# Kernel tuning notes

Hardware: AMD Instinct MI355X
Metric: run time of the kernel (lower is better)

The kernel has to match this reference:

```python
import jax, jax.numpy as jnp
import numpy as np

B, LQ, LK, D = 16, 2048, 2048, 64
TEMPERATURE = 8.0  # sqrt(d_k)


def setup_inputs() -> dict:
    key = jax.random.key(0)
    kq, kk, kv, km = jax.random.split(key, 4)
    q = jax.random.normal(kq, (B, LQ, D), dtype=jnp.float32)
    k = jax.random.normal(kk, (B, LK, D), dtype=jnp.float32)
    v = jax.random.normal(kv, (B, LK, D), dtype=jnp.float32)
    mask = jax.random.randint(km, (B, LQ, LK), 0, 2).astype(jnp.bool_)
    return {"q": q, "k": k, "v": v, "mask": mask}


def reference(q, k, v, mask):
    # attn = bmm(q, k^T) / temperature  -> [B, LQ, LK]
    attn = jnp.einsum("bqd,bkd->bqk", q, k) / TEMPERATURE
    attn = jnp.where(mask, -jnp.inf, attn)
    attn = jax.nn.softmax(attn, axis=2)
    out = jnp.einsum("bqk,bkd->bqd", attn, v)  # [B, LQ, D]
    return out, attn
```

## Files before the change

kernel.cpp:

```cpp
#include <hip/hip_runtime.h>
#include <hip/hip_bf16.h>

namespace {
constexpr int kB = 16;
constexpr int kLQ = 2048;
constexpr int kLK = 2048;
constexpr int kD = 64;
constexpr float kLog2e = 1.44269504088896340736f;
constexpr int kKStrB = 144;
constexpr int kMStrB = 136;
constexpr int kBStrB = 272;
constexpr int kChunk = 256;
constexpr int kEStrB = 528;
}

using short8 = __attribute__((ext_vector_type(8))) short;
using f32x4  = __attribute__((ext_vector_type(4))) float;

union S8U { short8 v; unsigned u[4]; };

static __device__ __forceinline__ unsigned pk2(float lo, float hi) {
    __hip_bfloat162 h = __float22bfloat162_rn(float2{lo, hi});
    unsigned short a = __builtin_bit_cast(unsigned short, h.x);
    unsigned short b = __builtin_bit_cast(unsigned short, h.y);
    return (unsigned)a | ((unsigned)b << 16);
}
static __device__ __forceinline__ float bf2f(unsigned short s) {
    unsigned u = ((unsigned)s) << 16;
    return __builtin_bit_cast(float, u);
}

__global__ __launch_bounds__(256, 6) void k1_fused(
    const float* __restrict__ qg, const float* __restrict__ kg,
    const void* __restrict__ maskg, unsigned short* __restrict__ ews,
    float* __restrict__ attng, float* __restrict__ outg)
{
    __shared__ __align__(16) unsigned char s_kst[128 * kKStrB];
    __shared__ __align__(16) unsigned char s_mst[16 * kMStrB];
    __shared__ __align__(16) unsigned char s_bnc[16 * kBStrB];
    __shared__ float s_wsum[4][16];
    __shared__ float s_rinv[16];
    __shared__ int s_flag;

    const int tid = threadIdx.x;
    const int wave = tid >> 6;
    const int lane = tid & 63;
    const int r16 = lane & 15;
    const int g = lane >> 4;

    const int blk = blockIdx.x;
    const int b = blk >> 7;
    const int qt = blk & 127;
    const size_t grow0 = (size_t)b * kLQ + qt * 16;

    if (tid < 64) {
        unsigned w = ((const unsigned*)maskg)[tid];
        unsigned long long bal = __ballot((w & 0xFFFFFF00u) != 0u);
        if (tid == 0) s_flag = (bal != 0ull) ? 1 : 0;
    }
    __syncthreads();
    const bool mask_byte = (s_flag != 0);
    const unsigned char* mask_u8 = (const unsigned char*)maskg;
    const int* mask_i32 = (const int*)maskg;

    short8 q0, q1;
    {
        const float4* qp = (const float4*)(qg + (grow0 + r16) * kD);
        const float s = 0.125f * kLog2e;
        float4 x0 = qp[2*g + 0], x1 = qp[2*g + 1];
        float4 x2 = qp[2*g + 8], x3 = qp[2*g + 9];
        x0 *= s; x1 *= s; x2 *= s; x3 *= s;
        S8U a, c;
        a.u[0] = pk2(x0.x, x0.y); a.u[1] = pk2(x0.z, x0.w);
        a.u[2] = pk2(x1.x, x1.y); a.u[3] = pk2(x1.z, x1.w);
        c.u[0] = pk2(x2.x, x2.y); c.u[1] = pk2(x2.z, x2.w);
        c.u[2] = pk2(x3.x, x3.y); c.u[3] = pk2(x3.z, x3.w);
        q0 = a.v; q1 = c.v;
    }

    float wsum = 0.f;

    for (int sub = 0; sub < kLK / 128; ++sub) {
        const int csub = sub * 128;
#pragma unroll
        for (int i = 0; i < 8; ++i) {
            const int row = (tid >> 4) + i * 16;
            const float4 y = *(const float4*)(kg + ((size_t)b * kLK + csub + row) * kD + (tid & 15) * 4);
            uint2 p{ pk2(y.x, y.y), pk2(y.z, y.w) };
            *(uint2*)(s_kst + row * kKStrB + (tid & 15) * 8) = p;
        }
        {
            const int mrow = tid >> 4;
            const int mseg = tid & 15;
            unsigned long long f;
            if (mask_byte) {
                f = *(const unsigned long long*)(mask_u8 + (grow0 + mrow) * kLK + csub + mseg * 8);
            } else {
                const int* mp = mask_i32 + (grow0 + mrow) * kLK + csub + mseg * 8;
                const int4 m0 = *(const int4*)mp;
                const int4 m1 = *(const int4*)(mp + 4);
                f  = (m0.x ? 1ull : 0ull)        | (m0.y ? 1ull << 8 : 0ull)
                   | (m0.z ? 1ull << 16 : 0ull)  | (m0.w ? 1ull << 24 : 0ull)
                   | (m1.x ? 1ull << 32 : 0ull)  | (m1.y ? 1ull << 40 : 0ull)
                   | (m1.z ? 1ull << 48 : 0ull)  | (m1.w ? 1ull << 56 : 0ull);
            }
            *(unsigned long long*)(s_mst + mrow * kMStrB + mseg * 8) = f;
        }
        __syncthreads();

        const unsigned char* kb = s_kst + (wave * 32 + r16) * kKStrB;
        const short8 kA0 = *(const short8*)(kb + g * 16);
        const short8 kA1 = *(const short8*)(kb + 64 + g * 16);
        const short8 kB0 = *(const short8*)(kb + 16 * kKStrB + g * 16);
        const short8 kB1 = *(const short8*)(kb + 16 * kKStrB + 64 + g * 16);
        f32x4 accA = {0.f, 0.f, 0.f, 0.f}, accB = {0.f, 0.f, 0.f, 0.f};
        accA = __builtin_amdgcn_mfma_f32_16x16x32_bf16(kA0, q0, accA, 0, 0, 0);
        accA = __builtin_amdgcn_mfma_f32_16x16x32_bf16(kA1, q1, accA, 0, 0, 0);
        accB = __builtin_amdgcn_mfma_f32_16x16x32_bf16(kB0, q0, accB, 0, 0, 0);
        accB = __builtin_amdgcn_mfma_f32_16x16x32_bf16(kB1, q1, accB, 0, 0, 0);

        const unsigned mwA = *(const unsigned*)(s_mst + r16 * kMStrB + wave * 32 + 4 * g);
        const unsigned mwB = *(const unsigned*)(s_mst + r16 * kMStrB + wave * 32 + 16 + 4 * g);
        float eA[4], eB[4];
#pragma unroll
        for (int r = 0; r < 4; ++r) {
            eA[r] = ((mwA >> (8*r)) & 0xFFu) ? 0.f : __builtin_amdgcn_exp2f(accA[r]);
            eB[r] = ((mwB >> (8*r)) & 0xFFu) ? 0.f : __builtin_amdgcn_exp2f(accB[r]);
        }
        wsum += (eA[0] + eA[1]) + (eA[2] + eA[3]) + (eB[0] + eB[1]) + (eB[2] + eB[3]);
        uint2 pA{ pk2(eA[0], eA[1]), pk2(eA[2], eA[3]) };
        uint2 pB{ pk2(eB[0], eB[1]), pk2(eB[2], eB[3]) };
        *(uint2*)(s_bnc + r16 * kBStrB + wave * 64 + 8 * g) = pA;
        *(uint2*)(s_bnc + r16 * kBStrB + wave * 64 + 32 + 8 * g) = pB;
        __syncthreads();

        {
            const int erow = tid >> 4;
            const int eseg = tid & 15;
            *(short8*)(ews + (grow0 + erow) * kLK + csub + eseg * 8) =
                *(const short8*)(s_bnc + erow * kBStrB + eseg * 16);
        }
    }

    wsum += __shfl_xor(wsum, 16, 64);
    wsum += __shfl_xor(wsum, 32, 64);
    if (g == 0) s_wsum[wave][r16] = wsum;
    __syncthreads();
    if (tid < 16) {
        const float rs = s_wsum[0][tid] + s_wsum[1][tid] + s_wsum[2][tid] + s_wsum[3][tid];
        outg[(grow0 + tid) * kD] = rs;
        s_rinv[tid] = __builtin_amdgcn_rcpf(rs);
    }
    __syncthreads();

#pragma unroll 2
    for (int r = 0; r < 16; ++r) {
        const float rinv = s_rinv[r];
        const short8 ev = *(const short8*)(ews + (grow0 + r) * kLK + tid * 8);
        f32x4 a0, a1;
        a0[0] = bf2f((unsigned short)ev[0]) * rinv;
        a0[1] = bf2f((unsigned short)ev[1]) * rinv;
        a0[2] = bf2f((unsigned short)ev[2]) * rinv;
        a0[3] = bf2f((unsigned short)ev[3]) * rinv;
        a1[0] = bf2f((unsigned short)ev[4]) * rinv;
        a1[1] = bf2f((unsigned short)ev[5]) * rinv;
        a1[2] = bf2f((unsigned short)ev[6]) * rinv;
        a1[3] = bf2f((unsigned short)ev[7]) * rinv;
        float* ap = attng + (grow0 + r) * kLK + tid * 8;
        *(f32x4*)ap = a0;
        *(f32x4*)(ap + 4) = a1;
    }
}

__global__ __launch_bounds__(512, 8) void k2_pv(
    const float* __restrict__ vg, const unsigned short* __restrict__ ews,
    float* __restrict__ outg)
{
    __shared__ __align__(16) unsigned char s_e[16 * kEStrB];
    __shared__ float s_red[16][kD];
    __shared__ float s_rinv[16];

    const int tid = threadIdx.x;
    const int wave = tid >> 6;
    const int lane = tid & 63;
    const int r16 = lane & 15;
    const int g = lane >> 4;

    const int blk = blockIdx.x;
    const int b = blk >> 7;
    const size_t grow0 = (size_t)b * kLQ + (blk & 127) * 16;

    if (tid < 16)
        s_rinv[tid] = __builtin_amdgcn_rcpf(outg[(grow0 + tid) * kD]);
    __syncthreads();

    const int d0 = (wave & 3) * 16;
    const int kh = wave >> 2;
    f32x4 acc = {0.f, 0.f, 0.f, 0.f};
    const float* vbase = vg + (size_t)b * kLK * kD + d0 + r16;

    for (int chunk = 0; chunk < kLK / kChunk; ++chunk) {
        const int c0 = chunk * kChunk;
        {
            const int row = tid >> 5;
            const int cc = tid & 31;
            const short8 ev = *(const short8*)(ews + (grow0 + row) * kLK + c0 + cc * 8);
            *(short8*)(s_e + row * kEStrB + cc * 16) = ev;
        }
        __syncthreads();
#pragma unroll
        for (int s = 0; s < 4; ++s) {
            const int kk = kh * 128 + s * 32 + 8 * g;
            const short8 af = *(const short8*)(s_e + r16 * kEStrB + kk * 2);
            const float* vp = vbase + (size_t)(c0 + kk) * kD;
            float v0 = vp[0*kD], v1 = vp[1*kD], v2 = vp[2*kD], v3 = vp[3*kD];
            float v4 = vp[4*kD], v5 = vp[5*kD], v6 = vp[6*kD], v7 = vp[7*kD];
            S8U bv;
            bv.u[0] = pk2(v0, v1); bv.u[1] = pk2(v2, v3);
            bv.u[2] = pk2(v4, v5); bv.u[3] = pk2(v6, v7);
            acc = __builtin_amdgcn_mfma_f32_16x16x32_bf16(af, bv.v, acc, 0, 0, 0);
        }
        __syncthreads();
    }

    if (kh == 1) {
#pragma unroll
        for (int r = 0; r < 4; ++r) s_red[4*g + r][d0 + r16] = acc[r];
    }
    __syncthreads();
    if (kh == 0) {
#pragma unroll
        for (int r = 0; r < 4; ++r) {
            const int m = 4*g + r;
            outg[(grow0 + m) * kD + d0 + r16] = (acc[r] + s_red[m][d0 + r16]) * s_rinv[m];
        }
    }
}

extern "C" void kernel_launch(void* const* d_in, const int* in_sizes, int n_in,
                              void* d_out, int out_size, void* d_ws, size_t ws_size,
                              hipStream_t stream) {
    (void)in_sizes; (void)n_in; (void)out_size; (void)ws_size;
    const float* q = (const float*)d_in[0];
    const float* k = (const float*)d_in[1];
    const float* v = (const float*)d_in[2];
    const void* mask = d_in[3];
    float* out = (float*)d_out;
    float* attn = out + (size_t)kB * kLQ * kD;
    unsigned short* ews = (unsigned short*)d_ws;
    k1_fused<<<dim3(kB * 128), 256, 0, stream>>>(q, k, mask, ews, attn, out);
    k2_pv<<<dim3(kB * 128), 512, 0, stream>>>(v, ews, out);
}
```

Measured before the change: 288.3 us.

## Fuse PV into score kernel, keeping exp row tile in shared memory

Result: slower. 364.5 us (+26.4%).

```diff
diff --git a/kernel.cpp b/kernel.cpp
--- a/kernel.cpp
+++ b/kernel.cpp
@@ -7,17 +7,15 @@
 constexpr int kLK = 2048;
 constexpr int kD = 64;
 constexpr float kLog2e = 1.44269504088896340736f;
+constexpr int kEStr = 2056;
 constexpr int kKStrB = 144;
-constexpr int kMStrB = 136;
-constexpr int kBStrB = 272;
-constexpr int kChunk = 256;
-constexpr int kEStrB = 528;
+constexpr int kMStrB = 72;
 }
 
 using short8 = __attribute__((ext_vector_type(8))) short;
 using f32x4  = __attribute__((ext_vector_type(4))) float;
 
-union S8U { short8 v; unsigned u[4]; };
+union S8U { short8 v; unsigned u[4]; unsigned long long q[2]; };
 
 static __device__ __forceinline__ unsigned pk2(float lo, float hi) {
     __hip_bfloat162 h = __float22bfloat162_rn(float2{lo, hi});
@@ -30,14 +28,14 @@
     return __builtin_bit_cast(float, u);
 }
 
-__global__ __launch_bounds__(256, 6) void k1_fused(
+__global__ __launch_bounds__(256, 2) void sdpa_fused(
     const float* __restrict__ qg, const float* __restrict__ kg,
-    const void* __restrict__ maskg, unsigned short* __restrict__ ews,
-    float* __restrict__ attng, float* __restrict__ outg)
+    const float* __restrict__ vg, const void* __restrict__ maskg,
+    float* __restrict__ outg, float* __restrict__ attng)
 {
-    __shared__ __align__(16) unsigned char s_kst[128 * kKStrB];
+    __shared__ unsigned short s_e[16][kEStr];
+    __shared__ __align__(16) unsigned char s_kst[64 * kKStrB];
     __shared__ __align__(16) unsigned char s_mst[16 * kMStrB];
-    __shared__ __align__(16) unsigned char s_bnc[16 * kBStrB];
     __shared__ float s_wsum[4][16];
     __shared__ float s_rinv[16];
     __shared__ int s_flag;
@@ -78,68 +76,74 @@
         q0 = a.v; q1 = c.v;
     }
 
+    const int srow = tid >> 4;
+    const int sseg = tid & 15;
+    const size_t kgbase = (size_t)b * kLK * kD;
+
+    float4 kpre0, kpre1, kpre2, kpre3;
+    unsigned mpre;
+    {
+        const float* kp = kg + kgbase + (size_t)srow * kD + sseg * 4;
+        kpre0 = *(const float4*)(kp + 0  * kD);
+        kpre1 = *(const float4*)(kp + 16 * kD);
+        kpre2 = *(const float4*)(kp + 32 * kD);
+        kpre3 = *(const float4*)(kp + 48 * kD);
+        if (mask_byte) {
+            mpre = *(const unsigned*)(mask_u8 + (grow0 + srow) * kLK + sseg * 4);
+        } else {
+            const int4 m = *(const int4*)(mask_i32 + (grow0 + srow) * kLK + sseg * 4);
+            mpre = (m.x ? 1u : 0u) | (m.y ? 0x100u : 0u) | (m.z ? 0x10000u : 0u) | (m.w ? 0x1000000u : 0u);
+        }
+    }
+
     float wsum = 0.f;
 
-    for (int sub = 0; sub < kLK / 128; ++sub) {
-        const int csub = sub * 128;
-#pragma unroll
-        for (int i = 0; i < 8; ++i) {
-            const int row = (tid >> 4) + i * 16;
-            const float4 y = *(const float4*)(kg + ((size_t)b * kLK + csub + row) * kD + (tid & 15) * 4);
-            uint2 p{ pk2(y.x, y.y), pk2(y.z, y.w) };
-            *(uint2*)(s_kst + row * kKStrB + (tid & 15) * 8) = p;
-        }
+    for (int sub = 0; sub < kLK / 64; ++sub) {
         {
-            const int mrow = tid >> 4;
-            const int mseg = tid & 15;
-            unsigned long long f;
+            uint2 p0{ pk2(kpre0.x, kpre0.y), pk2(kpre0.z, kpre0.w) };
+            uint2 p1{ pk2(kpre1.x, kpre1.y), pk2(kpre1.z, kpre1.w) };
+            uint2 p2{ pk2(kpre2.x, kpre2.y), pk2(kpre2.z, kpre2.w) };
+            uint2 p3{ pk2(kpre3.x, kpre3.y), pk2(kpre3.z, kpre3.w) };
+            *(uint2*)(s_kst + (srow +  0) * kKStrB + sseg * 8) = p0;
+            *(uint2*)(s_kst + (srow + 16) * kKStrB + sseg * 8) = p1;
+            *(uint2*)(s_kst + (srow + 32) * kKStrB + sseg * 8) = p2;
+            *(uint2*)(s_kst + (srow + 48) * kKStrB + sseg * 8) = p3;
+            *(unsigned*)(s_mst + srow * kMStrB + sseg * 4) = mpre;
+        }
+        __syncthreads();
+
+        if (sub + 1 < kLK / 64) {
+            const int csub = (sub + 1) * 64;
+            const float* kp = kg + kgbase + (size_t)(csub + srow) * kD + sseg * 4;
+            kpre0 = *(const float4*)(kp + 0  * kD);
+            kpre1 = *(const float4*)(kp + 16 * kD);
+            kpre2 = *(const float4*)(kp + 32 * kD);
+            kpre3 = *(const float4*)(kp + 48 * kD);
             if (mask_byte) {
-                f = *(const unsigned long long*)(mask_u8 + (grow0 + mrow) * kLK + csub + mseg * 8);
+                mpre = *(const unsigned*)(mask_u8 + (grow0 + srow) * kLK + csub + sseg * 4);
             } else {
-                const int* mp = mask_i32 + (grow0 + mrow) * kLK + csub + mseg * 8;
-                const int4 m0 = *(const int4*)mp;
-                const int4 m1 = *(const int4*)(mp + 4);
-                f  = (m0.x ? 1ull : 0ull)        | (m0.y ? 1ull << 8 : 0ull)
-                   | (m0.z ? 1ull << 16 : 0ull)  | (m0.w ? 1ull << 24 : 0ull)
-                   | (m1.x ? 1ull << 32 : 0ull)  | (m1.y ? 1ull << 40 : 0ull)
-                   | (m1.z ? 1ull << 48 : 0ull)  | (m1.w ? 1ull << 56 : 0ull);
+                const int4 m = *(const int4*)(mask_i32 + (grow0 + srow) * kLK + csub + sseg * 4);
+                mpre = (m.x ? 1u : 0u) | (m.y ? 0x100u : 0u) | (m.z ? 0x10000u : 0u) | (m.w ? 0x1000000u : 0u);
             }
-            *(unsigned long long*)(s_mst + mrow * kMStrB + mseg * 8) = f;
-        }
-        __syncthreads();
-
-        const unsigned char* kb = s_kst + (wave * 32 + r16) * kKStrB;
+        }
+
+        const unsigned char* kb = s_kst + (wave * 16 + r16) * kKStrB;
         const short8 kA0 = *(const short8*)(kb + g * 16);
         const short8 kA1 = *(const short8*)(kb + 64 + g * 16);
-        const short8 kB0 = *(const short8*)(kb + 16 * kKStrB + g * 16);
-        const short8 kB1 = *(const short8*)(kb + 16 * kKStrB + 64 + g * 16);
-        f32x4 accA = {0.f, 0.f, 0.f, 0.f}, accB = {0.f, 0.f, 0.f, 0.f};
-        accA = __builtin_amdgcn_mfma_f32_16x16x32_bf16(kA0, q0, accA, 0, 0, 0);
-        accA = __builtin_amdgcn_mfma_f32_16x16x32_bf16(kA1, q1, accA, 0, 0, 0);
-        accB = __builtin_amdgcn_mfma_f32_16x16x32_bf16(kB0, q0, accB, 0, 0, 0);
-        accB = __builtin_amdgcn_mfma_f32_16x16x32_bf16(kB1, q1, accB, 0, 0, 0);
-
-        const unsigned mwA = *(const unsigned*)(s_mst + r16 * kMStrB + wave * 32 + 4 * g);
-        const unsigned mwB = *(const unsigned*)(s_mst + r16 * kMStrB + wave * 32 + 16 + 4 * g);
-        float eA[4], eB[4];
+        f32x4 acc = {0.f, 0.f, 0.f, 0.f};
+        acc = __builtin_amdgcn_mfma_f32_16x16x32_bf16(kA0, q0, acc, 0, 0, 0);
+        acc = __builtin_amdgcn_mfma_f32_16x16x32_bf16(kA1, q1, acc, 0, 0, 0);
+
+        const unsigned mw = *(const unsigned*)(s_mst + r16 * kMStrB + wave * 16 + 4 * g);
+        float e4[4];
 #pragma unroll
-        for (int r = 0; r < 4; ++r) {
-            eA[r] = ((mwA >> (8*r)) & 0xFFu) ? 0.f : __builtin_amdgcn_exp2f(accA[r]);
-            eB[r] = ((mwB >> (8*r)) & 0xFFu) ? 0.f : __builtin_amdgcn_exp2f(accB[r]);
-        }
-        wsum += (eA[0] + eA[1]) + (eA[2] + eA[3]) + (eB[0] + eB[1]) + (eB[2] + eB[3]);
-        uint2 pA{ pk2(eA[0], eA[1]), pk2(eA[2], eA[3]) };
-        uint2 pB{ pk2(eB[0], eB[1]), pk2(eB[2], eB[3]) };
-        *(uint2*)(s_bnc + r16 * kBStrB + wave * 64 + 8 * g) = pA;
-        *(uint2*)(s_bnc + r16 * kBStrB + wave * 64 + 32 + 8 * g) = pB;
+        for (int r = 0; r < 4; ++r)
+            e4[r] = ((mw >> (8*r)) & 0xFFu) ? 0.f : __builtin_amdgcn_exp2f(acc[r]);
+        wsum += (e4[0] + e4[1]) + (e4[2] + e4[3]);
+        const unsigned long long pe = (unsigned long long)pk2(e4[0], e4[1])
+                                    | ((unsigned long long)pk2(e4[2], e4[3]) << 32);
+        *(unsigned long long*)&s_e[r16][sub * 64 + wave * 16 + 4 * g] = pe;
         __syncthreads();
-
-        {
-            const int erow = tid >> 4;
-            const int eseg = tid & 15;
-            *(short8*)(ews + (grow0 + erow) * kLK + csub + eseg * 8) =
-                *(const short8*)(s_bnc + erow * kBStrB + eseg * 16);
-        }
     }
 
     wsum += __shfl_xor(wsum, 16, 64);
@@ -148,7 +152,6 @@
     __syncthreads();
     if (tid < 16) {
         const float rs = s_wsum[0][tid] + s_wsum[1][tid] + s_wsum[2][tid] + s_wsum[3][tid];
-        outg[(grow0 + tid) * kD] = rs;
         s_rinv[tid] = __builtin_amdgcn_rcpf(rs);
     }
     __syncthreads();
@@ -156,7 +159,7 @@
 #pragma unroll 2
     for (int r = 0; r < 16; ++r) {
         const float rinv = s_rinv[r];
-        const short8 ev = *(const short8*)(ews + (grow0 + r) * kLK + tid * 8);
+        const short8 ev = *(const short8*)&s_e[r][tid * 8];
         f32x4 a0, a1;
         a0[0] = bf2f((unsigned short)ev[0]) * rinv;
         a0[1] = bf2f((unsigned short)ev[1]) * rinv;
@@ -166,73 +169,40 @@
         a1[1] = bf2f((unsigned short)ev[5]) * rinv;
         a1[2] = bf2f((unsigned short)ev[6]) * rinv;
         a1[3] = bf2f((unsigned short)ev[7]) * rinv;
-        float* ap = attng + (grow0 + r) * kLK + tid * 8;
+        float* ap = attng + (grow0 + r) * (size_t)kLK + tid * 8;
         *(f32x4*)ap = a0;
         *(f32x4*)(ap + 4) = a1;
     }
-}
-
-__global__ __launch_bounds__(512, 8) void k2_pv(
-    const float* __restrict__ vg, const unsigned short* __restrict__ ews,
-    float* __restrict__ outg)
-{
-    __shared__ __align__(16) unsigned char s_e[16 * kEStrB];
-    __shared__ float s_red[16][kD];
-    __shared__ float s_rinv[16];
-
-    const int tid = threadIdx.x;
-    const int wave = tid >> 6;
-    const int lane = tid & 63;
-    const int r16 = lane & 15;
-    const int g = lane >> 4;
-
-    const int blk = blockIdx.x;
-    const int b = blk >> 7;
-    const size_t grow0 = (size_t)b * kLQ + (blk & 127) * 16;
-
-    if (tid < 16)
-        s_rinv[tid] = __builtin_amdgcn_rcpf(outg[(grow0 + tid) * kD]);
-    __syncthreads();
-
-    const int d0 = (wave & 3) * 16;
-    const int kh = wave >> 2;
-    f32x4 acc = {0.f, 0.f, 0.f, 0.f};
-    const float* vbase = vg + (size_t)b * kLK * kD + d0 + r16;
-
-    for (int chunk = 0; chunk < kLK / kChunk; ++chunk) {
-        const int c0 = chunk * kChunk;
+
+    {
+        const int d0 = wave * 16;
+        const float* vbase = vg + (size_t)b * kLK * kD + d0 + r16;
+        float vp0, vp1, vp2, vp3, vp4, vp5, vp6, vp7;
         {
-            const int row = tid >> 5;
-            const int cc = tid & 31;
-            const short8 ev = *(const short8*)(ews + (grow0 + row) * kLK + c0 + cc * 8);
-            *(short8*)(s_e + row * kEStrB + cc * 16) = ev;
-        }
-        __syncthreads();
-#pragma unroll
-        for (int s = 0; s < 4; ++s) {
-            const int kk = kh * 128 + s * 32 + 8 * g;
-            const short8 af = *(const short8*)(s_e + r16 * kEStrB + kk * 2);
-            const float* vp = vbase + (size_t)(c0 + kk) * kD;
-            float v0 = vp[0*kD], v1 = vp[1*kD], v2 = vp[2*kD], v3 = vp[3*kD];
-            float v4 = vp[4*kD], v5 = vp[5*kD], v6 = vp[6*kD], v7 = vp[7*kD];
+            const float* vp = vbase + (size_t)(8 * g) * kD;
+            vp0 = vp[0*kD]; vp1 = vp[1*kD]; vp2 = vp[2*kD]; vp3 = vp[3*kD];
+            vp4 = vp[4*kD]; vp5 = vp[5*kD]; vp6 = vp[6*kD]; vp7 = vp[7*kD];
+        }
+        f32x4 acc = {0.f, 0.f, 0.f, 0.f};
+        for (int kt = 0; kt < kLK / 32; ++kt) {
+            const int kk0 = kt * 32 + 8 * g;
+            const float c0 = vp0, c1 = vp1, c2 = vp2, c3 = vp3;
+            const float c4 = vp4, c5 = vp5, c6 = vp6, c7 = vp7;
+            if (kt + 1 < kLK / 32) {
+                const float* vp = vbase + (size_t)(kk0 + 32) * kD;
+                vp0 = vp[0*kD]; vp1 = vp[1*kD]; vp2 = vp[2*kD]; vp3 = vp[3*kD];
+                vp4 = vp[4*kD]; vp5 = vp[5*kD]; vp6 = vp[6*kD]; vp7 = vp[7*kD];
+            }
+            const short8 af = *(const short8*)&s_e[r16][kk0];
             S8U bv;
-            bv.u[0] = pk2(v0, v1); bv.u[1] = pk2(v2, v3);
-            bv.u[2] = pk2(v4, v5); bv.u[3] = pk2(v6, v7);
+            bv.u[0] = pk2(c0, c1); bv.u[1] = pk2(c2, c3);
+            bv.u[2] = pk2(c4, c5); bv.u[3] = pk2(c6, c7);
             acc = __builtin_amdgcn_mfma_f32_16x16x32_bf16(af, bv.v, acc, 0, 0, 0);
         }
-        __syncthreads();
-    }
-
-    if (kh == 1) {
-#pragma unroll
-        for (int r = 0; r < 4; ++r) s_red[4*g + r][d0 + r16] = acc[r];
-    }
-    __syncthreads();
-    if (kh == 0) {
 #pragma unroll
         for (int r = 0; r < 4; ++r) {
-            const int m = 4*g + r;
-            outg[(grow0 + m) * kD + d0 + r16] = (acc[r] + s_red[m][d0 + r16]) * s_rinv[m];
+            const int m = 4 * g + r;
+            outg[(grow0 + m) * kD + d0 + r16] = acc[r] * s_rinv[m];
         }
     }
 }
@@ -240,14 +210,12 @@
 extern "C" void kernel_launch(void* const* d_in, const int* in_sizes, int n_in,
                               void* d_out, int out_size, void* d_ws, size_t ws_size,
                               hipStream_t stream) {
-    (void)in_sizes; (void)n_in; (void)out_size; (void)ws_size;
+    (void)in_sizes; (void)n_in; (void)out_size; (void)d_ws; (void)ws_size;
     const float* q = (const float*)d_in[0];
     const float* k = (const float*)d_in[1];
     const float* v = (const float*)d_in[2];
     const void* mask = d_in[3];
     float* out = (float*)d_out;
     float* attn = out + (size_t)kB * kLQ * kD;
-    unsigned short* ews = (unsigned short*)d_ws;
-    k1_fused<<<dim3(kB * 128), 256, 0, stream>>>(q, k, mask, ews, attn, out);
-    k2_pv<<<dim3(kB * 128), 512, 0, stream>>>(v, ews, out);
-}
+    sdpa_fused<<<dim3(kB * 128), 256, 0, stream>>>(q, k, v, mask, out, attn);
+}
```
